# Kernel tuning notes

Measured on AMD Instinct MI355X. Metric: run time of the kernel, lower is better.

Reference implementation:

```python
import jax, jax.numpy as jnp
import numpy as np

B = 131072
GI, GO = 4, 4          # input/output pathway groups
NI, NO = 64, 32        # neurons per input group (256/4), per output group (128/4)


def _gelu(t):
    # torch F.gelu default = exact erf gelu
    return jax.nn.gelu(t, approximate=False)


def setup_inputs() -> dict:
    key = jax.random.key(0)
    ks = jax.random.split(key, 16)
    s = 0.02
    return {
        "x":  jax.random.normal(ks[0], (B, 784), jnp.float32),
        "W1": jax.random.normal(ks[1], (512, 784), jnp.float32) * s,
        "b1": jax.random.normal(ks[2], (512,), jnp.float32) * s,
        "W2": jax.random.normal(ks[3], (256, 512), jnp.float32) * s,
        "b2": jax.random.normal(ks[4], (256,), jnp.float32) * s,
        "W3": jax.random.normal(ks[5], (128, 256), jnp.float32) * s,
        "b3": jax.random.normal(ks[6], (128,), jnp.float32) * s,
        "W4": jax.random.normal(ks[7], (64, 128), jnp.float32) * s,
        "b4": jax.random.normal(ks[8], (64,), jnp.float32) * s,
        "W5": jax.random.normal(ks[9], (32, 64), jnp.float32) * s,
        "b5": jax.random.normal(ks[10], (32,), jnp.float32) * s,
        "W6": jax.random.normal(ks[11], (10, 32), jnp.float32) * s,
        "b6": jax.random.normal(ks[12], (10,), jnp.float32) * s,
        "Wr": jax.random.normal(ks[13], (GI * GO, 256), jnp.float32) * s,
        "br": jax.random.normal(ks[14], (GI * GO,), jnp.float32) * s,
    }


def reference(x, W1, b1, W2, b2, W3, b3, W4, b4, W5, b5, W6, b6, Wr, br):
    # pre-middle dense chain (middle_layer == 3)
    h = _gelu(x @ W1.T + b1)          # [B, 512]
    mid_in = _gelu(h @ W2.T + b2)     # [B, 256]

    # router over 16 pathways; pathway_idx = i*GO + j -> reshape [B, GI, GO]
    pw = jax.nn.softmax(mid_in @ Wr.T + br, axis=-1).reshape(-1, GI, GO)

    # grouped pathway matmuls on fc3 (contiguous neuron groups -> reshape)
    xi = mid_in.reshape(-1, GI, NI)            # [B, GI, NI]
    W3g = W3.reshape(GO, NO, GI, NI)           # [GO, NO, GI, NI]
    part = jnp.einsum('bgi,ongi->bgon', xi, W3g)            # [B, GI, GO, NO]
    part = part + b3.reshape(GO, NO)[None, None]            # bias per pathway
    mid_out = jnp.einsum('bgo,bgon->bon', pw, part).reshape(-1, GO * NO)  # [B,128]
    mid_out = _gelu(mid_out)

    # post-middle dense chain
    h = _gelu(mid_out @ W4.T + b4)    # [B, 64]
    h = _gelu(h @ W5.T + b5)          # [B, 32]
    return h @ W6.T + b6              # [B, 10]
```

## Files before the change

### kernel.cpp

```cpp
#include <hip/hip_runtime.h>
#include <cstdint>

typedef _Float16 f16;
typedef _Float16 f16x4 __attribute__((ext_vector_type(4)));
typedef _Float16 f16x8 __attribute__((ext_vector_type(8)));
typedef float f32x4 __attribute__((ext_vector_type(4)));

#define MFMA16(a, b, c) __builtin_amdgcn_mfma_f32_16x16x32_f16((a), (b), (c), 0, 0, 0)

__device__ __forceinline__ float gelu_f(float x) {
    const float u = x * (1.5957691216f + 0.0713548163f * x * x);
    return x * __builtin_amdgcn_rcpf(1.0f + __expf(-u));
}

__device__ __forceinline__ void load_lds16(const void* g, void* l) {
    __builtin_amdgcn_global_load_lds(
        (const __attribute__((address_space(1))) void*)(uintptr_t)g,
        (__attribute__((address_space(3))) void*)(uint32_t)(uintptr_t)l,
        16, 0, 0);
}

__global__ void k_prep(const float* __restrict__ W1, const float* __restrict__ W2,
                       const float* __restrict__ W3, const float* __restrict__ W4,
                       const float* __restrict__ W5, const float* __restrict__ W6,
                       const float* __restrict__ Wr,
                       f16* __restrict__ W1p, f16* __restrict__ W2f, f16* __restrict__ W3f,
                       f16* __restrict__ W4f, f16* __restrict__ W5f, f16* __restrict__ W6p,
                       f16* __restrict__ Wrf) {
    int i = blockIdx.x * 256 + threadIdx.x;
    if (i < 425984) {
        int r = i / 832, c = i - r * 832;
        W1p[i] = (f16)(c < 784 ? W1[r * 784 + c] : 0.0f);
        return;
    }
    i -= 425984;
    if (i < 131072) { W2f[i] = (f16)W2[i]; return; }
    i -= 131072;
    if (i < 32768) { W3f[i] = (f16)W3[i]; return; }
    i -= 32768;
    if (i < 8192) { W4f[i] = (f16)W4[i]; return; }
    i -= 8192;
    if (i < 2048) { W5f[i] = (f16)W5[i]; return; }
    i -= 2048;
    if (i < 512) {
        int r = i >> 5, c = i & 31;
        W6p[i] = (f16)(r < 10 ? W6[r * 32 + c] : 0.0f);
        return;
    }
    i -= 512;
    if (i < 4096) { Wrf[i] = (f16)Wr[i]; return; }
}

__global__ __launch_bounds__(256)
void k_xcvt(const float* __restrict__ X, f16* __restrict__ X16) {
    const size_t t = (size_t)blockIdx.x * 256 + threadIdx.x;
    const size_t row = t / 208;
    const int c4 = (int)(t - row * 208) * 4;
    f16x4 v = {0, 0, 0, 0};
    if (c4 < 784) {
        const float4 f = *(const float4*)(X + row * 784 + c4);
        v[0] = (f16)f.x; v[1] = (f16)f.y; v[2] = (f16)f.z; v[3] = (f16)f.w;
    }
    *(f16x4*)(X16 + row * 832 + c4) = v;
}

__global__ __launch_bounds__(256, 2)
void k_gemm1(const f16* __restrict__ A, const f16* __restrict__ Bw,
             const float* __restrict__ bias, f16* __restrict__ C) {
    __shared__ f16 As[2 * 128 * 32];
    __shared__ f16 Bs[2 * 256 * 32];
    const int tid = threadIdx.x;
    const int wave = tid >> 6, lane = tid & 63;
    const int nt = blockIdx.x & 1;
    const size_t mt = blockIdx.x >> 1;
    const size_t row0 = mt * 128;
    const int col0 = nt * 256;
    const int am = lane & 15, akg = lane >> 4, ak = akg * 8;
    const int wm = (wave & 1) * 64, wn = (wave >> 1) * 128;
    const f32x4 zero4 = {0.f, 0.f, 0.f, 0.f};
    f32x4 acc[4][8];
#pragma unroll
    for (int i = 0; i < 4; ++i)
#pragma unroll
        for (int j = 0; j < 8; ++j) acc[i][j] = zero4;

    const int srow = lane >> 2;
    const int scol = (lane & 3) * 8;

    for (int kt = 0; kt < 13; ++kt) {
        const int kb = kt * 64;
#pragma unroll
        for (int p = 0; p < 2; ++p) {
#pragma unroll
            for (int i = 0; i < 2; ++i) {
                const int inst = wave * 2 + i;
                load_lds16(A + (row0 + inst * 16 + srow) * 832 + kb + p * 32 + scol,
                           &As[p * 4096 + inst * 512]);
            }
#pragma unroll
            for (int i = 0; i < 4; ++i) {
                const int inst = wave * 4 + i;
                load_lds16(Bw + (size_t)(col0 + inst * 16 + srow) * 832 + kb + p * 32 + scol,
                           &Bs[p * 8192 + inst * 512]);
            }
        }
        __syncthreads();
#pragma unroll
        for (int ks = 0; ks < 2; ++ks) {
            f16x8 af[4], bf[8];
#pragma unroll
            for (int i = 0; i < 4; ++i)
                af[i] = *(const f16x8*)&As[ks * 4096 + (wm + i * 16 + am) * 32 + ak];
#pragma unroll
            for (int j = 0; j < 8; ++j)
                bf[j] = *(const f16x8*)&Bs[ks * 8192 + (wn + j * 16 + am) * 32 + ak];
#pragma unroll
            for (int i = 0; i < 4; ++i)
#pragma unroll
                for (int j = 0; j < 8; ++j)
                    acc[i][j] = MFMA16(bf[j], af[i], acc[i][j]);
        }
        __syncthreads();
    }
    const int cc = akg * 4;
#pragma unroll
    for (int i = 0; i < 4; ++i) {
        const size_t row = row0 + wm + i * 16 + am;
#pragma unroll
        for (int j = 0; j < 8; ++j) {
            const int col = col0 + wn + j * 16 + cc;
            const float4 b4 = *(const float4*)(bias + col);
            f16x4 v;
            v[0] = (f16)gelu_f(acc[i][j][0] + b4.x);
            v[1] = (f16)gelu_f(acc[i][j][1] + b4.y);
            v[2] = (f16)gelu_f(acc[i][j][2] + b4.z);
            v[3] = (f16)gelu_f(acc[i][j][3] + b4.w);
            *(f16x4*)(C + row * 512 + col) = v;
        }
    }
}

__global__ __launch_bounds__(256, 2)
void k_gemm2(const f16* __restrict__ A, const f16* __restrict__ Bw,
             const float* __restrict__ bias, f16* __restrict__ C) {
    __shared__ f16 As[2 * 128 * 32];
    __shared__ f16 Bs[2 * 256 * 32];
    const int tid = threadIdx.x;
    const int wave = tid >> 6, lane = tid & 63;
    const size_t row0 = (size_t)blockIdx.x * 128;
    const int am = lane & 15, akg = lane >> 4, ak = akg * 8;
    const int wm = (wave & 1) * 64, wn = (wave >> 1) * 128;
    const f32x4 zero4 = {0.f, 0.f, 0.f, 0.f};
    f32x4 acc[4][8];
#pragma unroll
    for (int i = 0; i < 4; ++i)
#pragma unroll
        for (int j = 0; j < 8; ++j) acc[i][j] = zero4;

    const int srow = lane >> 2;
    const int scol = (lane & 3) * 8;

    for (int kt = 0; kt < 8; ++kt) {
        const int kb = kt * 64;
#pragma unroll
        for (int p = 0; p < 2; ++p) {
#pragma unroll
            for (int i = 0; i < 2; ++i) {
                const int inst = wave * 2 + i;
                load_lds16(A + (row0 + inst * 16 + srow) * 512 + kb + p * 32 + scol,
                           &As[p * 4096 + inst * 512]);
            }
#pragma unroll
            for (int i = 0; i < 4; ++i) {
                const int inst = wave * 4 + i;
                load_lds16(Bw + (size_t)(inst * 16 + srow) * 512 + kb + p * 32 + scol,
                           &Bs[p * 8192 + inst * 512]);
            }
        }
        __syncthreads();
#pragma unroll
        for (int ks = 0; ks < 2; ++ks) {
            f16x8 af[4], bf[8];
#pragma unroll
            for (int i = 0; i < 4; ++i)
                af[i] = *(const f16x8*)&As[ks * 4096 + (wm + i * 16 + am) * 32 + ak];
#pragma unroll
            for (int j = 0; j < 8; ++j)
                bf[j] = *(const f16x8*)&Bs[ks * 8192 + (wn + j * 16 + am) * 32 + ak];
#pragma unroll
            for (int i = 0; i < 4; ++i)
#pragma unroll
                for (int j = 0; j < 8; ++j)
                    acc[i][j] = MFMA16(bf[j], af[i], acc[i][j]);
        }
        __syncthreads();
    }
    const int cc = akg * 4;
#pragma unroll
    for (int i = 0; i < 4; ++i) {
        const size_t row = row0 + wm + i * 16 + am;
#pragma unroll
        for (int j = 0; j < 8; ++j) {
            const int col = wn + j * 16 + cc;
            const float4 b4 = *(const float4*)(bias + col);
            f16x4 v;
            v[0] = (f16)gelu_f(acc[i][j][0] + b4.x);
            v[1] = (f16)gelu_f(acc[i][j][1] + b4.y);
            v[2] = (f16)gelu_f(acc[i][j][2] + b4.z);
            v[3] = (f16)gelu_f(acc[i][j][3] + b4.w);
            *(f16x4*)(C + row * 256 + col) = v;
        }
    }
}

__global__ __launch_bounds__(256, 2)
void k_tail(const f16* __restrict__ MID,
            const f16* __restrict__ W3f, const float* __restrict__ b3,
            const f16* __restrict__ W4f, const float* __restrict__ b4,
            const f16* __restrict__ W5f, const float* __restrict__ b5,
            const f16* __restrict__ W6p, const float* __restrict__ b6v,
            const f16* __restrict__ Wrf, const float* __restrict__ brv,
            float* __restrict__ OUT) {
    __shared__ f16 s_mid[64 * 264];
    __shared__ float s_pw[64 * 20];
    __shared__ f16 s_mo[64 * 136];
    __shared__ f16 s_h4[64 * 72];
    __shared__ f16 s_h5[64 * 40];
    const int tid = threadIdx.x, wave = tid >> 6, lane = tid & 63;
    const size_t r0 = (size_t)blockIdx.x * 64;
    const int am = lane & 15, akg = lane >> 4, ak = akg * 8;
    const int wr = wave * 16;
    const int crow = wr + akg * 4;
    const f32x4 zero4 = {0.f, 0.f, 0.f, 0.f};

    {
        const int row = tid >> 2, seg = (tid & 3) * 64;
        const f16* src = MID + (r0 + row) * 256 + seg;
        f16* dst = s_mid + row * 264 + seg;
#pragma unroll
        for (int c = 0; c < 8; ++c)
            *(f16x8*)(dst + c * 8) = *(const f16x8*)(src + c * 8);
    }
    __syncthreads();

    {
        f32x4 lacc = zero4;
#pragma unroll
        for (int ks = 0; ks < 8; ++ks) {
            f16x8 a = *(const f16x8*)(s_mid + (wr + am) * 264 + ks * 32 + ak);
            f16x8 b = *(const f16x8*)(Wrf + am * 256 + ks * 32 + ak);
            lacc = MFMA16(a, b, lacc);
        }
        const float brn = brv[am];
#pragma unroll
        for (int r = 0; r < 4; ++r) {
            float l = lacc[r] + brn;
            float mx = l;
#pragma unroll
            for (int m = 1; m <= 8; m <<= 1) mx = fmaxf(mx, __shfl_xor(mx, m));
            const float e = __expf(l - mx);
            float s = e;
#pragma unroll
            for (int m = 1; m <= 8; m <<= 1) s += __shfl_xor(s, m);
            const float p = e / s;
            float sg = p;
            sg += __shfl_xor(sg, 4);
            sg += __shfl_xor(sg, 8);
            s_pw[(crow + r) * 20 + am] = p;
            if (am < 4) s_pw[(crow + r) * 20 + 16 + am] = sg;
        }
    }
    __syncthreads();

    {
        f16x8 a3[4][2];
#pragma unroll
        for (int g = 0; g < 4; ++g)
#pragma unroll
            for (int kh = 0; kh < 2; ++kh)
                a3[g][kh] = *(const f16x8*)(s_mid + (wr + am) * 264 + g * 64 + kh * 32 + ak);
#pragma unroll
        for (int o = 0; o < 4; ++o) {
            float pwv[4][4], sgl[4];
#pragma unroll
            for (int r = 0; r < 4; ++r) {
                sgl[r] = s_pw[(crow + r) * 20 + 16 + o];
#pragma unroll
                for (int g = 0; g < 4; ++g)
                    pwv[g][r] = s_pw[(crow + r) * 20 + g * 4 + o];
            }
#pragma unroll
            for (int ctl = 0; ctl < 2; ++ctl) {
                const int ct = o * 2 + ctl;
                const int col = ct * 16 + am;
                const float bias = b3[col];
                f32x4 oacc;
#pragma unroll
                for (int r = 0; r < 4; ++r) oacc[r] = bias * sgl[r];
#pragma unroll
                for (int g = 0; g < 4; ++g) {
                    f32x4 t = zero4;
                    t = MFMA16(a3[g][0], *(const f16x8*)(W3f + (size_t)col * 256 + g * 64 + ak), t);
                    t = MFMA16(a3[g][1], *(const f16x8*)(W3f + (size_t)col * 256 + g * 64 + 32 + ak), t);
#pragma unroll
                    for (int r = 0; r < 4; ++r) oacc[r] += pwv[g][r] * t[r];
                }
#pragma unroll
                for (int r = 0; r < 4; ++r)
                    s_mo[(crow + r) * 136 + col] = (f16)gelu_f(oacc[r]);
            }
        }
    }
    __syncthreads();

    {
        f16x8 a4[4];
#pragma unroll
        for (int ks = 0; ks < 4; ++ks)
            a4[ks] = *(const f16x8*)(s_mo + (wr + am) * 136 + ks * 32 + ak);
#pragma unroll
        for (int ct = 0; ct < 4; ++ct) {
            const int col = ct * 16 + am;
            f32x4 acc = zero4;
#pragma unroll
            for (int ks = 0; ks < 4; ++ks)
                acc = MFMA16(a4[ks], *(const f16x8*)(W4f + (size_t)col * 128 + ks * 32 + ak), acc);
            const float bias = b4[col];
#pragma unroll
            for (int r = 0; r < 4; ++r)
                s_h4[(crow + r) * 72 + col] = (f16)gelu_f(acc[r] + bias);
        }
    }
    __syncthreads();

    {
        f16x8 a5[2];
#pragma unroll
        for (int ks = 0; ks < 2; ++ks)
            a5[ks] = *(const f16x8*)(s_h4 + (wr + am) * 72 + ks * 32 + ak);
#pragma unroll
        for (int ct = 0; ct < 2; ++ct) {
            const int col = ct * 16 + am;
            f32x4 acc = zero4;
#pragma unroll
            for (int ks = 0; ks < 2; ++ks)
                acc = MFMA16(a5[ks], *(const f16x8*)(W5f + (size_t)col * 64 + ks * 32 + ak), acc);
            const float bias = b5[col];
#pragma unroll
            for (int r = 0; r < 4; ++r)
                s_h5[(crow + r) * 40 + col] = (f16)gelu_f(acc[r] + bias);
        }
    }
    __syncthreads();

    {
        f16x8 a6 = *(const f16x8*)(s_h5 + (wr + am) * 40 + ak);
        f16x8 bw = *(const f16x8*)(W6p + am * 32 + ak);
        f32x4 acc = MFMA16(a6, bw, zero4);
        if (am < 10) {
            const float bb = b6v[am];
#pragma unroll
            for (int r = 0; r < 4; ++r)
                OUT[(r0 + crow + r) * 10 + am] = acc[r] + bb;
        }
    }
}

extern "C" void kernel_launch(void* const* d_in, const int* in_sizes, int n_in,
                              void* d_out, int out_size, void* d_ws, size_t ws_size,
                              hipStream_t stream) {
    const float* x  = (const float*)d_in[0];
    const float* W1 = (const float*)d_in[1];
    const float* b1 = (const float*)d_in[2];
    const float* W2 = (const float*)d_in[3];
    const float* b2 = (const float*)d_in[4];
    const float* W3 = (const float*)d_in[5];
    const float* b3 = (const float*)d_in[6];
    const float* W4 = (const float*)d_in[7];
    const float* b4 = (const float*)d_in[8];
    const float* W5 = (const float*)d_in[9];
    const float* b5 = (const float*)d_in[10];
    const float* W6 = (const float*)d_in[11];
    const float* b6 = (const float*)d_in[12];
    const float* Wr = (const float*)d_in[13];
    const float* br = (const float*)d_in[14];
    float* out = (float*)d_out;

    const int M = in_sizes[0] / 784;

    char* ws = (char*)d_ws;
    f16* W1p = (f16*)ws; ws += 512 * 832 * 2;
    f16* W2f = (f16*)ws; ws += 256 * 512 * 2;
    f16* W3f = (f16*)ws; ws += 128 * 256 * 2;
    f16* W4f = (f16*)ws; ws += 64 * 128 * 2;
    f16* W5f = (f16*)ws; ws += 32 * 64 * 2;
    f16* W6p = (f16*)ws; ws += 16 * 32 * 2;
    f16* Wrf = (f16*)ws; ws += 16 * 256 * 2;
    f16* X16 = (f16*)ws;
    f16* MIDB = (f16*)ws; ws += (size_t)M * 832 * 2;
    f16* H1  = (f16*)ws; ws += (size_t)M * 512 * 2;

    k_prep<<<2362, 256, 0, stream>>>(W1, W2, W3, W4, W5, W6, Wr,
                                     W1p, W2f, W3f, W4f, W5f, W6p, Wrf);
    k_xcvt<<<(M * 208) / 256, 256, 0, stream>>>(x, X16);
    k_gemm1<<<(M / 128) * 2, 256, 0, stream>>>(X16, W1p, b1, H1);
    k_gemm2<<<M / 128, 256, 0, stream>>>(H1, W2f, b2, MIDB);
    k_tail<<<M / 64, 256, 0, stream>>>(MIDB, W3f, b3, W4f, b4, W5f, b5,
                                       W6p, b6, Wrf, br, out);
}
```

Measured before the change: 906.5 us.

## Fuse fp32-to-fp16 input conversion into first GEMM and drop tail kernel barriers

Removes the separate x conversion kernel. gemm1 now reads fp32 x directly from global memory into registers and converts it to fp16 fragments, so the f16 copy of x is never written or re-read. The tail kernel is restructured so each wave stages only its own 16 rows into shared memory, which lets every __syncthreads be dropped. The cost is that A-tile loads in gemm1 become uncached, per-lane global reads. Each x element is also fetched by both N-tile blocks and by the two waves sharing a row range, with no LDS reuse.

```diff
diff --git a/kernel.cpp b/kernel.cpp
--- a/kernel.cpp
+++ b/kernel.cpp
@@ -51,23 +51,9 @@
     if (i < 4096) { Wrf[i] = (f16)Wr[i]; return; }
 }
 
-__global__ __launch_bounds__(256)
-void k_xcvt(const float* __restrict__ X, f16* __restrict__ X16) {
-    const size_t t = (size_t)blockIdx.x * 256 + threadIdx.x;
-    const size_t row = t / 208;
-    const int c4 = (int)(t - row * 208) * 4;
-    f16x4 v = {0, 0, 0, 0};
-    if (c4 < 784) {
-        const float4 f = *(const float4*)(X + row * 784 + c4);
-        v[0] = (f16)f.x; v[1] = (f16)f.y; v[2] = (f16)f.z; v[3] = (f16)f.w;
-    }
-    *(f16x4*)(X16 + row * 832 + c4) = v;
-}
-
 __global__ __launch_bounds__(256, 2)
-void k_gemm1(const f16* __restrict__ A, const f16* __restrict__ Bw,
+void k_gemm1(const float* __restrict__ A, const f16* __restrict__ Bw,
              const float* __restrict__ bias, f16* __restrict__ C) {
-    __shared__ f16 As[2 * 128 * 32];
     __shared__ f16 Bs[2 * 256 * 32];
     const int tid = threadIdx.x;
     const int wave = tid >> 6, lane = tid & 63;
@@ -78,6 +64,7 @@
     const int am = lane & 15, akg = lane >> 4, ak = akg * 8;
     const int wm = (wave & 1) * 64, wn = (wave >> 1) * 128;
     const f32x4 zero4 = {0.f, 0.f, 0.f, 0.f};
+    const f16x8 zero8 = {0, 0, 0, 0, 0, 0, 0, 0};
     f32x4 acc[4][8];
 #pragma unroll
     for (int i = 0; i < 4; ++i)
@@ -91,12 +78,6 @@
         const int kb = kt * 64;
 #pragma unroll
         for (int p = 0; p < 2; ++p) {
-#pragma unroll
-            for (int i = 0; i < 2; ++i) {
-                const int inst = wave * 2 + i;
-                load_lds16(A + (row0 + inst * 16 + srow) * 832 + kb + p * 32 + scol,
-                           &As[p * 4096 + inst * 512]);
-            }
 #pragma unroll
             for (int i = 0; i < 4; ++i) {
                 const int inst = wave * 4 + i;
@@ -104,13 +85,29 @@
                            &Bs[p * 8192 + inst * 512]);
             }
         }
+        f16x8 af[2][4];
+#pragma unroll
+        for (int ks = 0; ks < 2; ++ks) {
+#pragma unroll
+            for (int i = 0; i < 4; ++i) {
+                const int c = kb + ks * 32 + ak;
+                if (c < 784) {
+                    const float* p = A + (row0 + wm + i * 16 + am) * 784 + c;
+                    const float4 lo = *(const float4*)p;
+                    const float4 hi = *(const float4*)(p + 4);
+                    f16x8 v;
+                    v[0] = (f16)lo.x; v[1] = (f16)lo.y; v[2] = (f16)lo.z; v[3] = (f16)lo.w;
+                    v[4] = (f16)hi.x; v[5] = (f16)hi.y; v[6] = (f16)hi.z; v[7] = (f16)hi.w;
+                    af[ks][i] = v;
+                } else {
+                    af[ks][i] = zero8;
+                }
+            }
+        }
         __syncthreads();
 #pragma unroll
         for (int ks = 0; ks < 2; ++ks) {
-            f16x8 af[4], bf[8];
-#pragma unroll
-            for (int i = 0; i < 4; ++i)
-                af[i] = *(const f16x8*)&As[ks * 4096 + (wm + i * 16 + am) * 32 + ak];
+            f16x8 bf[8];
 #pragma unroll
             for (int j = 0; j < 8; ++j)
                 bf[j] = *(const f16x8*)&Bs[ks * 8192 + (wn + j * 16 + am) * 32 + ak];
@@ -118,7 +115,7 @@
             for (int i = 0; i < 4; ++i)
 #pragma unroll
                 for (int j = 0; j < 8; ++j)
-                    acc[i][j] = MFMA16(bf[j], af[i], acc[i][j]);
+                    acc[i][j] = MFMA16(bf[j], af[ks][i], acc[i][j]);
         }
         __syncthreads();
     }
@@ -234,14 +231,13 @@
     const f32x4 zero4 = {0.f, 0.f, 0.f, 0.f};
 
     {
-        const int row = tid >> 2, seg = (tid & 3) * 64;
+        const int row = wr + (lane >> 2), seg = (lane & 3) * 64;
         const f16* src = MID + (r0 + row) * 256 + seg;
         f16* dst = s_mid + row * 264 + seg;
 #pragma unroll
         for (int c = 0; c < 8; ++c)
             *(f16x8*)(dst + c * 8) = *(const f16x8*)(src + c * 8);
     }
-    __syncthreads();
 
     {
         f32x4 lacc = zero4;
@@ -270,7 +266,6 @@
             if (am < 4) s_pw[(crow + r) * 20 + 16 + am] = sg;
         }
     }
-    __syncthreads();
 
     {
         f16x8 a3[4][2];
@@ -311,7 +306,6 @@
             }
         }
     }
-    __syncthreads();
 
     {
         f16x8 a4[4];
@@ -331,7 +325,6 @@
                 s_h4[(crow + r) * 72 + col] = (f16)gelu_f(acc[r] + bias);
         }
     }
-    __syncthreads();
 
     {
         f16x8 a5[2];
@@ -351,7 +344,6 @@
                 s_h5[(crow + r) * 40 + col] = (f16)gelu_f(acc[r] + bias);
         }
     }
-    __syncthreads();
 
     {
         f16x8 a6 = *(const f16x8*)(s_h5 + (wr + am) * 40 + ak);
@@ -396,14 +388,12 @@
     f16* W5f = (f16*)ws; ws += 32 * 64 * 2;
     f16* W6p = (f16*)ws; ws += 16 * 32 * 2;
     f16* Wrf = (f16*)ws; ws += 16 * 256 * 2;
-    f16* X16 = (f16*)ws;
-    f16* MIDB = (f16*)ws; ws += (size_t)M * 832 * 2;
     f16* H1  = (f16*)ws; ws += (size_t)M * 512 * 2;
+    f16* MIDB= (f16*)ws; ws += (size_t)M * 256 * 2;
 
     k_prep<<<2362, 256, 0, stream>>>(W1, W2, W3, W4, W5, W6, Wr,
                                      W1p, W2f, W3f, W4f, W5f, W6p, Wrf);
-    k_xcvt<<<(M * 208) / 256, 256, 0, stream>>>(x, X16);
-    k_gemm1<<<(M / 128) * 2, 256, 0, stream>>>(X16, W1p, b1, H1);
+    k_gemm1<<<(M / 128) * 2, 256, 0, stream>>>(x, W1p, b1, H1);
     k_gemm2<<<M / 128, 256, 0, stream>>>(H1, W2f, b2, MIDB);
     k_tail<<<M / 64, 256, 0, stream>>>(MIDB, W3f, b3, W4f, b4, W5f, b5,
                                        W6p, b6, Wrf, br, out);
```

After: 883.5 us. -2.5%, faster.
